# Kernel optimization log

Hardware: AMD Instinct MI355X
Metric: run time of the kernel (lower is better)

## Reference

```python
import jax, jax.numpy as jnp
import numpy as np

LMBDA = 100.0
GAMMA = 0.5  # resolvant_gamma


def setup_inputs() -> dict:
    key = jax.random.key(0)
    ks = jax.random.split(key, 8)
    B, Vx, Vy, C, K = 1, 5000, 5000, 128, 64
    feat_x = jax.random.normal(ks[0], (B, Vx, C), dtype=jnp.float32)
    feat_y = jax.random.normal(ks[1], (B, Vy, C), dtype=jnp.float32)
    # positive, sorted eigenvalues (Laplacian spectrum)
    evals_x = jnp.sort(jax.random.uniform(ks[2], (B, K), minval=0.01, maxval=10.0), axis=-1)
    evals_y = jnp.sort(jax.random.uniform(ks[3], (B, K), minval=0.01, maxval=10.0), axis=-1)
    # pseudo-inverse eigenvector rows, scaled ~1/sqrt(V) for realistic magnitudes
    evecs_trans_x = jax.random.normal(ks[4], (B, K, Vx), dtype=jnp.float32) / np.sqrt(Vx)
    evecs_trans_y = jax.random.normal(ks[5], (B, K, Vy), dtype=jnp.float32) / np.sqrt(Vy)
    # sqrt mass matrices: well-conditioned near-identity (must be invertible)
    eye = jnp.eye(K, dtype=jnp.float32)
    sqrtMk_x = eye[None] + 0.05 * jax.random.normal(ks[6], (B, K, K), dtype=jnp.float32)
    sqrtMk_y = eye[None] + 0.05 * jax.random.normal(ks[7], (B, K, K), dtype=jnp.float32)
    return {
        "feat_x": feat_x, "feat_y": feat_y,
        "evals_x": evals_x, "evals_y": evals_y,
        "evecs_trans_x": evecs_trans_x, "evecs_trans_y": evecs_trans_y,
        "sqrtMk_x": sqrtMk_x, "sqrtMk_y": sqrtMk_y,
    }


def _compute_fmap(fx, fy, ex, ey, Px, Py, Mx, My):
    # fx:[V,C] fy:[V,C] ex,ey:[K] Px,Py:[K,V] Mx,My:[K,K]
    A = Px @ fx                 # [K,C] spectral coeffs of source feats
    Bc = My @ (Py @ fy)         # adapt_feature=True: [K,C]
    k, m = A.shape
    vec_B = Bc.T.reshape(m * k, 1)
    # Ik = sqrtMk_y (adapt_feature, no dev_feature)
    At_Ik = jnp.kron(A.T, My)   # [m*k, k*k]
    first = At_Ik.T @ At_Ik     # [k*k, k*k]
    # adapt_mask=True branch: resolvent mask as Kronecker operators
    inv_Mx = jnp.linalg.inv(Mx)
    s = jnp.maximum(jnp.max(ex), jnp.max(ey))
    g1 = (ex / s) ** GAMMA
    g2 = (ey / s) ** GAMMA
    rn1_re = g1 / (g1 * g1 + 1.0)
    rn1_im = 1.0 / (g1 * g1 + 1.0)
    rn2_re = g2 / (g2 * g2 + 1.0)
    rn2_im = 1.0 / (g2 * g2 + 1.0)
    lx_re = jnp.kron(rn1_re[:, None] * inv_Mx, My)          # diag(rn1_re)@inv_Mx
    lx_im = jnp.kron(rn1_im[:, None] * inv_Mx, My)
    ly_re = jnp.kron(inv_Mx, My * rn2_re[None, :])          # My@diag(rn2_re)
    ly_im = jnp.kron(inv_Mx, My * rn2_im[None, :])
    D_re = ly_re - lx_re
    D_im = ly_im - lx_im
    second = D_re.T @ D_re + D_im.T @ D_im
    rhs = At_Ik.T @ vec_B
    op = first + LMBDA * second
    C = jnp.linalg.solve(op, rhs).reshape(k, k).T
    return C[None]  # [1,K,K]


def reference(feat_x, feat_y, evals_x, evals_y, evecs_trans_x, evecs_trans_y, sqrtMk_x, sqrtMk_y):
    Cxy = _compute_fmap(
        feat_x[0], feat_y[0], evals_x[0], evals_y[0],
        evecs_trans_x[0], evecs_trans_y[0], sqrtMk_x[0], sqrtMk_y[0],
    )
    return Cxy  # bidirectional=False -> Cyx is None
```

## Files before the change

### kernel.cpp

```cpp
#include <hip/hip_runtime.h>

#define NV 5000
#define LMB 100.0f
#define MAXIT 150
#define TOL 1e-10f
#define NBLK 16
#define NALL 96
#define BSZ 512

#define SV_O     0
#define CTRL_O   256
#define PART_O   2048
#define AH_O     657408
#define B0_O     665600
#define H_O      673792
#define E_O      677888
#define Z2_O     681984
#define ZH_O     686080
#define Q0_O     690176
#define LIH_O    702464
#define LIE_O    706560
#define U0_O     710656
#define LH_O     747520
#define BT_O     751616
#define RSTK_O   755712
#define LCT_O    772096
#define WG_O     788480
#define XG_O     792576
#define WS_NEED  796672

#define MS_O     PART_O
#define PRT2_O   (PART_O + 16384)
#define ZERO_N   26048

#define LCTS_S   0
#define RPK_S    12288
#define TPART_S  13312
#define TPACK_S  19552
#define SPART_S  20320
#define SM_FLOATS 22368

typedef unsigned long long u64;
union PKu { u64 u; float2 f; };

__device__ __forceinline__ float aload(const float* p) {
  return __hip_atomic_load(p, __ATOMIC_RELAXED, __HIP_MEMORY_SCOPE_AGENT);
}
__device__ __forceinline__ void astore(float* p, float v) {
  __hip_atomic_store(p, v, __ATOMIC_RELAXED, __HIP_MEMORY_SCOPE_AGENT);
}
__device__ __forceinline__ u64 aload64(const u64* p) {
  return __hip_atomic_load(p, __ATOMIC_RELAXED, __HIP_MEMORY_SCOPE_AGENT);
}
__device__ __forceinline__ void astore64(u64* p, u64 v) {
  __hip_atomic_store(p, v, __ATOMIC_RELAXED, __HIP_MEMORY_SCOPE_AGENT);
}

__device__ __forceinline__ void gbar(int* cnt, int target) {
  __syncthreads();
  if (threadIdx.x == 0) {
    __hip_atomic_fetch_add(cnt, 1, __ATOMIC_ACQ_REL, __HIP_MEMORY_SCOPE_AGENT);
    while (__hip_atomic_load(cnt, __ATOMIC_ACQUIRE, __HIP_MEMORY_SCOPE_AGENT) < target) {
      __builtin_amdgcn_s_sleep(2);
    }
  }
  __syncthreads();
}

__device__ __forceinline__ void stageN(float* dst, const float* src) {
  for (int e = threadIdx.x; e < 4096; e += BSZ)
    dst[(e >> 6) * 65 + (e & 63)] = src[e];
}
__device__ __forceinline__ void stageT(float* dst, const float* src) {
  for (int e = threadIdx.x; e < 4096; e += BSZ)
    dst[(e & 63) * 65 + (e >> 6)] = src[e];
}
__device__ __forceinline__ void mm65(const float* Ls, const float* Rs, float* D) {
  for (int e = threadIdx.x; e < 4096; e += BSZ) {
    int i = e >> 6, j = e & 63;
    float a0 = 0.f, a1 = 0.f;
#pragma unroll 8
    for (int t = 0; t < 64; t += 2) {
      a0 = fmaf(Ls[i * 65 + t], Rs[t * 65 + j], a0);
      a1 = fmaf(Ls[i * 65 + t + 1], Rs[(t + 1) * 65 + j], a1);
    }
    D[e] = a0 + a1;
  }
}
__device__ __forceinline__ void mm65L(const float* Ls, const float* Rs, float* DL) {
  for (int e = threadIdx.x; e < 4096; e += BSZ) {
    int i = e >> 6, j = e & 63;
    float a0 = 0.f, a1 = 0.f;
#pragma unroll 8
    for (int t = 0; t < 64; t += 2) {
      a0 = fmaf(Ls[i * 65 + t], Rs[t * 65 + j], a0);
      a1 = fmaf(Ls[i * 65 + t + 1], Rs[(t + 1) * 65 + j], a1);
    }
    DL[i * 65 + j] = a0 + a1;
  }
}
__device__ void mmNN_s(const float* L, const float* R, float* D, float* sm) {
  stageN(sm, L); stageN(sm + 4160, R);
  __syncthreads();
  mm65(sm, sm + 4160, D);
}

__device__ void chol_inv(const float* S, float* Li, float* Lf, float* sm) {
  float (*M)[65] = (float (*)[65])sm;
  float (*T)[65] = (float (*)[65])(sm + 64 * 65);
  int tid = threadIdx.x;
  for (int e = tid; e < 4096; e += BSZ) {
    M[e >> 6][e & 63] = S[e];
    T[e >> 6][e & 63] = 0.f;
  }
  __syncthreads();
  for (int j = 0; j < 64; ++j) {
    float pv = M[j][j];
    __syncthreads();
    float sc = rsqrtf(pv);
    if (tid < 64 - j) M[j + tid][j] *= sc;
    __syncthreads();
    int m = 63 - j, c2 = (m * (m + 1)) >> 1;
    for (int e = tid; e < c2; e += BSZ) {
      int rp = (int)((sqrtf(8.f * (float)e + 1.f) - 1.f) * 0.5f);
      while (((rp + 1) * (rp + 2)) >> 1 <= e) ++rp;
      while ((rp * (rp + 1)) >> 1 > e) --rp;
      int cp = e - ((rp * (rp + 1)) >> 1);
      int r = j + 1 + rp, c = j + 1 + cp;
      M[r][c] = fmaf(-M[r][j], M[c][j], M[r][c]);
    }
    __syncthreads();
  }
  if (tid < 64) {
    int c = tid;
    T[c][c] = 1.f / M[c][c];
    for (int r = c + 1; r < 64; ++r) {
      float s = 0.f;
      for (int t = c; t < r; ++t) s = fmaf(M[r][t], T[t][c], s);
      T[r][c] = -s / M[r][r];
    }
  }
  __syncthreads();
  if (Lf) {
    for (int e = tid; e < 4096; e += BSZ) {
      int r = e >> 6, c = e & 63;
      Lf[e] = (r >= c) ? M[r][c] : 0.f;
    }
  }
  for (int e = tid; e < 4096; e += BSZ) Li[e] = T[e >> 6][e & 63];
}

__device__ __forceinline__ float coop_apply8(float* sm, const float* yv, float y_own,
                                             int lane, int wv8) {
  const float* LCTs = sm + LCTS_S;
  const float* Rpk = sm + RPK_S;
  float* Tpart = sm + TPART_S;
  float* Tpack = sm + TPACK_S;
  float* Spart = sm + SPART_S;
  float t1p[12];
#pragma unroll
  for (int p = 0; p < 12; ++p) t1p[p] = 0.f;
#pragma unroll
  for (int u = 0; u < 8; ++u) {
    int m = u * 8 + wv8;
    float yu = yv[u];
    float4 rA = *(const float4*)&Rpk[m * 16 + 0];
    float4 rB = *(const float4*)&Rpk[m * 16 + 4];
    float4 rC = *(const float4*)&Rpk[m * 16 + 8];
    t1p[0] = fmaf(yu, rA.x, t1p[0]);  t1p[1] = fmaf(yu, rA.y, t1p[1]);
    t1p[2] = fmaf(yu, rA.z, t1p[2]);  t1p[3] = fmaf(yu, rA.w, t1p[3]);
    t1p[4] = fmaf(yu, rB.x, t1p[4]);  t1p[5] = fmaf(yu, rB.y, t1p[5]);
    t1p[6] = fmaf(yu, rB.z, t1p[6]);  t1p[7] = fmaf(yu, rB.w, t1p[7]);
    t1p[8] = fmaf(yu, rC.x, t1p[8]);  t1p[9] = fmaf(yu, rC.y, t1p[9]);
    t1p[10] = fmaf(yu, rC.z, t1p[10]); t1p[11] = fmaf(yu, rC.w, t1p[11]);
  }
#pragma unroll
  for (int p = 0; p < 12; ++p) Tpart[wv8 * 780 + p * 65 + lane] = t1p[p];
  __syncthreads();
  int tid = wv8 * 64 + lane;
  for (int z = tid; z < 768; z += BSZ) {
    int tk = z >> 2, c = z & 3;
    int p = (tk >> 6) * 4 + c, k = tk & 63;
    float s = ((Tpart[0 * 780 + p * 65 + k] + Tpart[1 * 780 + p * 65 + k]) +
               (Tpart[2 * 780 + p * 65 + k] + Tpart[3 * 780 + p * 65 + k])) +
              ((Tpart[4 * 780 + p * 65 + k] + Tpart[5 * 780 + p * 65 + k]) +
               (Tpart[6 * 780 + p * 65 + k] + Tpart[7 * 780 + p * 65 + k]));
    Tpack[z] = s;
  }
  __syncthreads();
  float s0 = 0.f, s1 = 0.f, s2 = 0.f, s3 = 0.f;
  int tk0 = wv8 * 24;
#pragma unroll 8
  for (int q = 0; q < 24; ++q) {
    int tk = tk0 + q;
    float lv = LCTs[tk * 64 + lane];
    float4 tv = *(const float4*)&Tpack[tk * 4];
    s0 = fmaf(lv, tv.x, s0);
    s1 = fmaf(lv, tv.y, s1);
    s2 = fmaf(lv, tv.z, s2);
    s3 = fmaf(lv, tv.w, s3);
  }
  Spart[wv8 * 256 + 0 * 64 + lane] = s0;
  Spart[wv8 * 256 + 1 * 64 + lane] = s1;
  Spart[wv8 * 256 + 2 * 64 + lane] = s2;
  Spart[wv8 * 256 + 3 * 64 + lane] = s3;
  __syncthreads();
  int cw = (wv8 & 3) * 64 + lane;
  return y_own + (((Spart[0 * 256 + cw] + Spart[1 * 256 + cw]) +
                   (Spart[2 * 256 + cw] + Spart[3 * 256 + cw])) +
                  ((Spart[4 * 256 + cw] + Spart[5 * 256 + cw]) +
                   (Spart[6 * 256 + cw] + Spart[7 * 256 + cw])));
}

__global__ __launch_bounds__(BSZ) void solve_kernel(const float* fx, const float* fy,
                                                    const float* ex, const float* ey,
                                                    const float* Px, const float* Py,
                                                    const float* Mx, const float* My,
                                                    float* W, float* out) {
  __shared__ float sm[SM_FLOATS] __attribute__((aligned(16)));
  __shared__ float sLd[192], sRd[192], wred[8], scal[2];
  int tid = threadIdx.x, blk = blockIdx.x;
  int* cnt = (int*)(W + CTRL_O);

  if (blk < 80) {
    int mat = (blk >= 40), seg = mat ? (blk - 40) : blk;
    const float* P = (mat ? Py : Px);
    const float* f = (mat ? fy : fx);
    int v0 = seg * 125;
    for (int e = tid; e < 8000; e += BSZ) {
      int rr = e / 125, vv = e - rr * 125;
      sm[rr * 126 + vv] = P[rr * NV + v0 + vv];
    }
    __syncthreads();
    int rg = (tid >> 5) << 2;
    int cq = (tid & 31) << 2;
    float acc[4][4];
#pragma unroll
    for (int u = 0; u < 4; ++u)
#pragma unroll
      for (int v = 0; v < 4; ++v) acc[u][v] = 0.f;
    for (int v5 = 0; v5 < 125; v5 += 5) {
      float4 fv[5];
#pragma unroll
      for (int q = 0; q < 5; ++q)
        fv[q] = *(const float4*)(f + (size_t)(v0 + v5 + q) * 128 + cq);
#pragma unroll
      for (int q = 0; q < 5; ++q) {
#pragma unroll
        for (int u = 0; u < 4; ++u) {
          float pv = sm[(rg + u) * 126 + v5 + q];
          acc[u][0] = fmaf(pv, fv[q].x, acc[u][0]);
          acc[u][1] = fmaf(pv, fv[q].y, acc[u][1]);
          acc[u][2] = fmaf(pv, fv[q].z, acc[u][2]);
          acc[u][3] = fmaf(pv, fv[q].w, acc[u][3]);
        }
      }
    }
    float* O = W + PART_O + (size_t)blk * 8192;
#pragma unroll
    for (int u = 0; u < 4; ++u) {
      float4 o = make_float4(acc[u][0], acc[u][1], acc[u][2], acc[u][3]);
      *(float4*)(O + (rg + u) * 128 + cq) = o;
    }
  } else if (blk < 82) {
    for (int e = tid; e < 4096; e += BSZ) sm[(e >> 6) * 65 + (e & 63)] = My[e];
    __syncthreads();
    int base = (blk - 80) * 2048;
    for (int e = tid; e < 2048; e += BSZ) {
      int i = (base + e) >> 6, j = (base + e) & 63;
      float a0 = 0.f, a1 = 0.f;
#pragma unroll 8
      for (int t = 0; t < 64; t += 2) {
        a0 = fmaf(sm[t * 65 + i], sm[t * 65 + j], a0);
        a1 = fmaf(sm[(t + 1) * 65 + i], sm[(t + 1) * 65 + j], a1);
      }
      W[H_O + base + e] = a0 + a1;
    }
  } else if (blk == 82) {
    if (tid < 64) {
      float vx = ex[tid], vy = ey[tid];
      float m = fmaxf(vx, vy);
#pragma unroll
      for (int o = 32; o > 0; o >>= 1) m = fmaxf(m, __shfl_xor(m, o, 64));
      float g1 = sqrtf(vx / m), g2 = sqrtf(vy / m);
      float d1 = 1.f / fmaf(g1, g1, 1.f), d2 = 1.f / fmaf(g2, g2, 1.f);
      W[SV_O + tid] = g1 * d1;
      W[SV_O + 64 + tid] = d1;
      W[SV_O + 128 + tid] = g2 * d2;
      W[SV_O + 192 + tid] = d2;
    }
  }
  gbar(cnt, NALL);
  if (blk >= NBLK) return;

  if (blk == 0) {
    chol_inv(W + H_O, W + LIH_O, W + LH_O, sm);
  } else {
    for (int item = blk; item < 20; item += 15) {
      if (item <= 8) {
        int c0 = (item - 1) * 16;
        float* ssum = sm;
        float* mxs = sm + 1088;
        for (int e = tid; e < 4096; e += BSZ) mxs[(e >> 6) * 65 + (e & 63)] = Mx[e];
        for (int e = tid; e < 1024; e += BSZ) {
          int t = e >> 4, cl = e & 15;
          float s = 0.f;
          for (int p = 0; p < 40; ++p) s += W[PART_O + (size_t)p * 8192 + t * 128 + c0 + cl];
          ssum[t * 17 + cl] = s;
        }
        __syncthreads();
        for (int e = tid; e < 1024; e += BSZ) {
          int i = e >> 4, cl = e & 15;
          float a0 = 0.f, a1 = 0.f;
#pragma unroll 8
          for (int t = 0; t < 64; t += 2) {
            a0 = fmaf(mxs[t * 65 + i], ssum[t * 17 + cl], a0);
            a1 = fmaf(mxs[(t + 1) * 65 + i], ssum[(t + 1) * 17 + cl], a1);
          }
          W[AH_O + i * 128 + c0 + cl] = a0 + a1;
        }
      } else if (item <= 16) {
        int base = (item - 9) * 1024;
        for (int e = tid; e < 1024; e += BSZ) {
          float s = 0.f;
          for (int p = 0; p < 40; ++p) s += W[PART_O + (size_t)(40 + p) * 8192 + base + e];
          W[B0_O + base + e] = s;
        }
      } else {
        if (tid < 256) sm[tid] = W[SV_O + tid];
        __syncthreads();
        int t = item - 17;
        for (int e = tid; e < 4096; e += BSZ) {
          int k = e >> 6, b = e & 63;
          float h = W[H_O + e], v;
          if (t == 0) v = h * (sm[128 + k] * sm[128 + b] + sm[192 + k] * sm[192 + b]);
          else if (t == 1) v = h * (sm[128 + k] + sm[128 + b]);
          else v = h * (sm[192 + k] + sm[192 + b]);
          W[Q0_O + t * 4096 + e] = v;
        }
      }
      __syncthreads();
    }
  }
  gbar(cnt, NALL + NBLK);

  if (blk < 4) {
    for (int e = tid; e < 8192; e += BSZ) {
      int i = e >> 7, c = e & 127;
      sm[c * 65 + i] = W[AH_O + e];
    }
    __syncthreads();
    int i0 = blk * 16;
    for (int e = tid; e < 1024; e += BSZ) {
      int i = i0 + (e >> 6), j = e & 63;
      float a0 = 0.f, a1 = 0.f;
#pragma unroll 8
      for (int c = 0; c < 128; c += 2) {
        a0 = fmaf(sm[c * 65 + i], sm[c * 65 + j], a0);
        a1 = fmaf(sm[(c + 1) * 65 + i], sm[(c + 1) * 65 + j], a1);
      }
      float acc = a0 + a1;
      if (i == j) {
        float a = W[SV_O + i], b = W[SV_O + 64 + i];
        acc += LMB * (a * a + b * b);
      }
      W[E_O + i * 64 + j] = acc;
    }
  } else if (blk < 8) {
    int i0 = (blk - 4) * 16;
    for (int e = tid; e < 8192; e += BSZ) {
      int j = e >> 7, c = e & 127;
      sm[c * 65 + j] = W[B0_O + e];
    }
    for (int e = tid; e < 2048; e += BSZ) {
      int il = e >> 7, c = e & 127;
      sm[8320 + c * 17 + il] = W[AH_O + (i0 + il) * 128 + c];
    }
    __syncthreads();
    for (int e = tid; e < 1024; e += BSZ) {
      int il = e >> 6, j = e & 63;
      float a0 = 0.f, a1 = 0.f;
#pragma unroll 8
      for (int c = 0; c < 128; c += 2) {
        a0 = fmaf(sm[8320 + c * 17 + il], sm[c * 65 + j], a0);
        a1 = fmaf(sm[8320 + (c + 1) * 17 + il], sm[(c + 1) * 65 + j], a1);
      }
      W[Z2_O + (i0 + il) * 64 + j] = a0 + a1;
    }
  } else if (blk < 11) {
    int t = blk - 8;
    mmNN_s(W + LIH_O, W + Q0_O + t * 4096, W + U0_O + t * 4096, sm);
  } else {
    for (int e = (blk - 11) * BSZ + tid; e < ZERO_N; e += 5 * BSZ)
      W[MS_O + e] = 0.f;
  }
  gbar(cnt, NALL + 2 * NBLK);

  if (blk == 0) chol_inv(W + E_O, W + LIE_O, nullptr, sm);
  else if (blk == 1) mmNN_s(W + Z2_O, W + LH_O, W + ZH_O, sm);
  else if (blk < 5) {
    int t = blk - 2;
    stageN(sm, W + U0_O + t * 4096);
    stageT(sm + 4160, W + LIH_O);
    __syncthreads();
    mm65L(sm, sm + 4160, sm + 8320);
    __syncthreads();
    for (int e = tid; e < 4096; e += BSZ) {
      int a = e >> 6, b = e & 63;
      W[RSTK_O + t * 4096 + e] = 0.5f * (sm[8320 + a * 65 + b] + sm[8320 + b * 65 + a]);
    }
  }
  gbar(cnt, NALL + 3 * NBLK);

  if (blk == 0) mmNN_s(W + LIE_O, W + ZH_O, W + BT_O, sm);
  else if (blk == 1) {
    stageN(sm, W + LIE_O);
    stageT(sm + 4160, W + LIE_O);
    __syncthreads();
    mm65L(sm, sm + 4160, sm + 8320);
    __syncthreads();
    for (int e = tid; e < 4096; e += BSZ) {
      int k = e >> 6, i = e & 63;
      W[LCT_O + e] = LMB * 0.5f * (sm[8320 + k * 65 + i] + sm[8320 + i * 65 + k]);
    }
  } else if (blk < 4) {
    float* dv = sLd;
    if (tid < 64) dv[tid] = W[SV_O + ((blk == 2) ? tid : 64 + tid)];
    stageN(sm, W + LIE_O);
    __syncthreads();
    for (int e = tid; e < 4096; e += BSZ) {
      int jq = e >> 6, k = e & 63;
      sm[4160 + k * 65 + jq] = sm[jq * 65 + k] * dv[k];
    }
    __syncthreads();
    mm65L(sm, sm + 4160, sm + 8320);
    __syncthreads();
    int t = blk - 1;
    for (int e = tid; e < 4096; e += BSZ) {
      int k = e >> 6, i = e & 63;
      W[LCT_O + t * 4096 + e] = -LMB * 0.5f * (sm[8320 + k * 65 + i] + sm[8320 + i * 65 + k]);
    }
  }
  gbar(cnt, NALL + 4 * NBLK);

  int lane = tid & 63, wv8 = tid >> 6;
  int jown = blk * 4 + (wv8 & 3);
  const float* BTp = W + BT_O;
  const float* LCTp = W + LCT_O;
  const float* RSTKp = W + RSTK_O;
  u64* MS = (u64*)(W + MS_O);
  u64* PR2 = (u64*)(W + PRT2_O);

  for (int e = tid; e < 12288; e += BSZ) sm[LCTS_S + e] = LCTp[e];
  for (int e = tid; e < 768; e += BSZ) {
    int p = e >> 6, m = e & 63;
    int t = p >> 2, c = p & 3;
    sm[RPK_S + m * 16 + p] = RSTKp[(t * 64 + blk * 4 + c) * 64 + m];
  }
  if (tid < 192) {
    int t = tid >> 6, i = tid & 63;
    sLd[tid] = LCTp[t * 4096 + i * 64 + i];
    sRd[tid] = RSTKp[t * 4096 + i * 64 + i];
  }
  __syncthreads();
  float yv0[8];
#pragma unroll
  for (int u = 0; u < 8; ++u) {
    int col = u * 8 + wv8;
    float den = 1.f + sLd[lane] * sRd[col] + sLd[64 + lane] * sRd[64 + col] +
                sLd[128 + lane] * sRd[128 + col];
    yv0[u] = BTp[lane * 64 + col] / den;
  }
  float invd = 0.f, u_l = 0.f, r_l = 0.f, m_l = 0.f;
  if (wv8 < 4) {
    invd = 1.f / (1.f + sLd[lane] * sRd[jown] + sLd[64 + lane] * sRd[64 + jown] +
                  sLd[128 + lane] * sRd[128 + jown]);
    u_l = BTp[lane * 64 + jown] * invd;
    r_l = BTp[lane * 64 + jown];
  }
  float w_l = coop_apply8(sm, yv0, u_l, lane, wv8);
  if (wv8 < 4) {
    m_l = invd * w_l;
    PKu pk; pk.f = make_float2(m_l, 1.f);
    astore64(MS + jown * 64 + lane, pk.u);
    float vr = r_l * u_l, vw = w_l * u_l;
#pragma unroll
    for (int o = 32; o; o >>= 1) { vr += __shfl_down(vr, o, 64); vw += __shfl_down(vw, o, 64); }
    if (lane == 0) { wred[wv8 * 2] = vr; wred[wv8 * 2 + 1] = vw; }
  }
  __syncthreads();
  if (tid == 0) {
    PKu a, b;
    a.f = make_float2(wred[0] + wred[2] + wred[4] + wred[6], 1.f);
    b.f = make_float2(wred[1] + wred[3] + wred[5] + wred[7], 1.f);
    astore64(PR2 + (size_t)blk * 2, a.u);
    astore64(PR2 + (size_t)blk * 2 + 1, b.u);
  }

  float p_l = 0.f, q_l = 0.f, z_l = 0.f, s_l = 0.f, x_l = 0.f;
  float gprev = 1.f, aprev = 1.f, g0b = 1.f;
  int sl = lane & 15;
  for (int j = 0; j < MAXIT; ++j) {
    unsigned sbits = __float_as_uint((float)(j + 1));
    const u64* msrc = MS + (size_t)(j & 1) * 4096;
    u64 raw[8];
#pragma unroll
    for (int u = 0; u < 8; ++u) raw[u] = aload64(msrc + u * BSZ + tid);
    const u64* ps = PR2 + ((size_t)j * 16 + sl) * 2;
    u64 ra = 0, rb = 0;
    if (wv8 == 0) { ra = aload64(ps); rb = aload64(ps + 1); }
    {
      int spins = 0;
      for (;;) {
        bool ok = true;
#pragma unroll
        for (int u = 0; u < 8; ++u) ok = ok && ((unsigned)(raw[u] >> 32) == sbits);
        if (__all(ok)) break;
        if (++spins > 64) {
          __hip_atomic_load(msrc + tid, __ATOMIC_ACQUIRE, __HIP_MEMORY_SCOPE_AGENT);
          spins = 0;
        }
#pragma unroll
        for (int u = 0; u < 8; ++u)
          if ((unsigned)(raw[u] >> 32) != sbits) raw[u] = aload64(msrc + u * BSZ + tid);
      }
    }
    float mv[8];
#pragma unroll
    for (int u = 0; u < 8; ++u) mv[u] = __uint_as_float((unsigned)raw[u]);
    float n_l = coop_apply8(sm, mv, m_l, lane, wv8);
    if (wv8 == 0) {
      int spins = 0;
      for (;;) {
        bool ok = ((unsigned)(ra >> 32) == sbits) && ((unsigned)(rb >> 32) == sbits);
        if (__all(ok)) break;
        if (++spins > 64) {
          __hip_atomic_load(ps, __ATOMIC_ACQUIRE, __HIP_MEMORY_SCOPE_AGENT);
          spins = 0;
        }
        if ((unsigned)(ra >> 32) != sbits) ra = aload64(ps);
        if ((unsigned)(rb >> 32) != sbits) rb = aload64(ps + 1);
      }
      float pr = __uint_as_float((unsigned)ra), pw = __uint_as_float((unsigned)rb);
#pragma unroll
      for (int mm = 1; mm < 16; mm <<= 1) {
        pr += __shfl_xor(pr, mm, 64);
        pw += __shfl_xor(pw, mm, 64);
      }
      if (lane == 0) { scal[0] = pr; scal[1] = pw; }
    }
    __syncthreads();
    float gjb = scal[0], djb = scal[1];
    if (j == 0) g0b = gjb;
    if (j > 0 && fabsf(gjb) < TOL * fabsf(g0b)) break;
    if (wv8 < 4) {
      float bj = (j == 0) ? 0.f : gjb / gprev;
      float aj = (j == 0) ? gjb / djb : gjb / (djb - bj * gjb / aprev);
      float z_n = fmaf(bj, z_l, n_l);
      float w_n = fmaf(-aj, z_n, w_l);
      float m_n = invd * w_n;
      PKu pk; pk.f = make_float2(m_n, (float)(j + 2));
      astore64(MS + (size_t)((j + 1) & 1) * 4096 + jown * 64 + lane, pk.u);
      q_l = fmaf(bj, q_l, m_l);
      s_l = fmaf(bj, s_l, w_l);
      p_l = fmaf(bj, p_l, u_l);
      x_l = fmaf(aj, p_l, x_l);
      r_l = fmaf(-aj, s_l, r_l);
      u_l = fmaf(-aj, q_l, u_l);
      z_l = z_n; w_l = w_n; m_l = m_n;
      float vr = r_l * u_l, vw = w_l * u_l;
#pragma unroll
      for (int o = 32; o; o >>= 1) { vr += __shfl_down(vr, o, 64); vw += __shfl_down(vw, o, 64); }
      if (lane == 0) { wred[wv8 * 2] = vr; wred[wv8 * 2 + 1] = vw; }
      gprev = gjb; aprev = aj;
    }
    __syncthreads();
    if (tid == 0) {
      PKu a, b;
      a.f = make_float2(wred[0] + wred[2] + wred[4] + wred[6], (float)(j + 2));
      b.f = make_float2(wred[1] + wred[3] + wred[5] + wred[7], (float)(j + 2));
      astore64(PR2 + ((size_t)(j + 1) * 16 + blk) * 2, a.u);
      astore64(PR2 + ((size_t)(j + 1) * 16 + blk) * 2 + 1, b.u);
    }
  }
  if (wv8 < 4) astore(W + XG_O + jown * 64 + lane, x_l);
  gbar(cnt, NALL + 5 * NBLK);

  if (blk == 0) {
    float* Ys = sm;
    float* Ms2 = sm + 4160;
    for (int e = tid; e < 4096; e += BSZ) Ys[(e >> 6) * 65 + (e & 63)] = aload(W + XG_O + e);
    for (int e = tid; e < 4096; e += BSZ) Ms2[(e >> 6) * 65 + (e & 63)] = W[LIE_O + e];
    __syncthreads();
    for (int e = tid; e < 4096; e += BSZ) {
      int t = e >> 6, b = e & 63;
      float acc = 0.f;
#pragma unroll 8
      for (int a = 0; a < 64; ++a) acc = fmaf(Ms2[a * 65 + t], Ys[b * 65 + a], acc);
      W[WG_O + t * 64 + b] = acc;
    }
    __syncthreads();
    for (int e = tid; e < 4096; e += BSZ) Ys[(e >> 6) * 65 + (e & 63)] = W[WG_O + e];
    for (int e = tid; e < 4096; e += BSZ) Ms2[(e >> 6) * 65 + (e & 63)] = W[LIH_O + e];
    __syncthreads();
    for (int e = tid; e < 4096; e += BSZ) {
      int t = e >> 6, c = e & 63;
      float acc = 0.f;
#pragma unroll 8
      for (int b = 0; b < 64; ++b) acc = fmaf(Ys[t * 65 + b], Ms2[b * 65 + c], acc);
      W[WG_O + t * 64 + c] = acc;
    }
    __syncthreads();
    for (int e = tid; e < 4096; e += BSZ) Ys[(e >> 6) * 65 + (e & 63)] = W[WG_O + e];
    for (int e = tid; e < 4096; e += BSZ) Ms2[(e & 63) * 65 + (e >> 6)] = Mx[e];
    __syncthreads();
    for (int e = tid; e < 4096; e += BSZ) {
      int r = e >> 6, c = e & 63;
      float acc = 0.f;
#pragma unroll 8
      for (int t = 0; t < 64; ++t) acc = fmaf(Ms2[t * 65 + c], Ys[t * 65 + r], acc);
      out[e] = acc;
    }
  }
}

extern "C" void kernel_launch(void* const* d_in, const int* in_sizes, int n_in,
                              void* d_out, int out_size, void* d_ws, size_t ws_size,
                              hipStream_t stream) {
  const float* fx = (const float*)d_in[0];
  const float* fy = (const float*)d_in[1];
  const float* ex = (const float*)d_in[2];
  const float* ey = (const float*)d_in[3];
  const float* Px = (const float*)d_in[4];
  const float* Py = (const float*)d_in[5];
  const float* Mx = (const float*)d_in[6];
  const float* My = (const float*)d_in[7];
  float* out = (float*)d_out;
  float* W = (float*)d_ws;

  if (ws_size < (size_t)WS_NEED * sizeof(float)) {
    hipMemsetAsync(d_out, 0, (size_t)out_size * sizeof(float), stream);
    return;
  }

  hipMemsetAsync(W + CTRL_O, 0, 256, stream);
  solve_kernel<<<NALL, BSZ, 0, stream>>>(fx, fy, ex, ey, Px, Py, Mx, My, W, out);
}
```

Baseline: 353.1 us.

## Split iterative solver across 32 blocks with two columns per block

Doubles the number of blocks in the iterative CG-style solve phase from 16 to 32. Each block now owns 2 columns of the 64x64 unknown instead of 4, so the per-iteration operator apply shrinks. The shared-memory staging, the partial-reduction slots and the preprocessing item assignment are resized to match. The cost is more blocks taking part in each per-iteration cross-block flag exchange and reduction, which lengthens the synchronization and polling path that dominates each iteration.

```diff
diff --git a/kernel.cpp b/kernel.cpp
--- a/kernel.cpp
+++ b/kernel.cpp
@@ -4,7 +4,7 @@
 #define LMB 100.0f
 #define MAXIT 150
 #define TOL 1e-10f
-#define NBLK 16
+#define NBLK 32
 #define NALL 96
 #define BSZ 512
 
@@ -31,14 +31,14 @@
 
 #define MS_O     PART_O
 #define PRT2_O   (PART_O + 16384)
-#define ZERO_N   26048
+#define ZERO_N   35712
 
 #define LCTS_S   0
 #define RPK_S    12288
-#define TPART_S  13312
-#define TPACK_S  19552
-#define SPART_S  20320
-#define SM_FLOATS 22368
+#define TPART_S  12800
+#define TPACK_S  15920
+#define SPART_S  16304
+#define SM_FLOATS 21504
 
 typedef unsigned long long u64;
 union PKu { u64 u; float2 f; };
@@ -150,66 +150,57 @@
   for (int e = tid; e < 4096; e += BSZ) Li[e] = T[e >> 6][e & 63];
 }
 
-__device__ __forceinline__ float coop_apply8(float* sm, const float* yv, float y_own,
-                                             int lane, int wv8) {
+__device__ __forceinline__ float coop_apply(float* sm, const float* yv, float y_own,
+                                            int lane, int wv8) {
   const float* LCTs = sm + LCTS_S;
   const float* Rpk = sm + RPK_S;
   float* Tpart = sm + TPART_S;
   float* Tpack = sm + TPACK_S;
   float* Spart = sm + SPART_S;
-  float t1p[12];
-#pragma unroll
-  for (int p = 0; p < 12; ++p) t1p[p] = 0.f;
+  float t1p[6];
+#pragma unroll
+  for (int p = 0; p < 6; ++p) t1p[p] = 0.f;
 #pragma unroll
   for (int u = 0; u < 8; ++u) {
     int m = u * 8 + wv8;
     float yu = yv[u];
-    float4 rA = *(const float4*)&Rpk[m * 16 + 0];
-    float4 rB = *(const float4*)&Rpk[m * 16 + 4];
-    float4 rC = *(const float4*)&Rpk[m * 16 + 8];
+    float4 rA = *(const float4*)&Rpk[m * 8 + 0];
+    float2 rB = *(const float2*)&Rpk[m * 8 + 4];
     t1p[0] = fmaf(yu, rA.x, t1p[0]);  t1p[1] = fmaf(yu, rA.y, t1p[1]);
     t1p[2] = fmaf(yu, rA.z, t1p[2]);  t1p[3] = fmaf(yu, rA.w, t1p[3]);
     t1p[4] = fmaf(yu, rB.x, t1p[4]);  t1p[5] = fmaf(yu, rB.y, t1p[5]);
-    t1p[6] = fmaf(yu, rB.z, t1p[6]);  t1p[7] = fmaf(yu, rB.w, t1p[7]);
-    t1p[8] = fmaf(yu, rC.x, t1p[8]);  t1p[9] = fmaf(yu, rC.y, t1p[9]);
-    t1p[10] = fmaf(yu, rC.z, t1p[10]); t1p[11] = fmaf(yu, rC.w, t1p[11]);
-  }
-#pragma unroll
-  for (int p = 0; p < 12; ++p) Tpart[wv8 * 780 + p * 65 + lane] = t1p[p];
+  }
+#pragma unroll
+  for (int p = 0; p < 6; ++p) Tpart[wv8 * 390 + p * 65 + lane] = t1p[p];
   __syncthreads();
   int tid = wv8 * 64 + lane;
-  for (int z = tid; z < 768; z += BSZ) {
-    int tk = z >> 2, c = z & 3;
-    int p = (tk >> 6) * 4 + c, k = tk & 63;
-    float s = ((Tpart[0 * 780 + p * 65 + k] + Tpart[1 * 780 + p * 65 + k]) +
-               (Tpart[2 * 780 + p * 65 + k] + Tpart[3 * 780 + p * 65 + k])) +
-              ((Tpart[4 * 780 + p * 65 + k] + Tpart[5 * 780 + p * 65 + k]) +
-               (Tpart[6 * 780 + p * 65 + k] + Tpart[7 * 780 + p * 65 + k]));
-    Tpack[z] = s;
-  }
-  __syncthreads();
-  float s0 = 0.f, s1 = 0.f, s2 = 0.f, s3 = 0.f;
+  if (tid < 384) {
+    int tk = tid >> 1, c = tid & 1;
+    int p = (tk >> 6) * 2 + c, k = tk & 63;
+    Tpack[tid] = (((Tpart[0 * 390 + p * 65 + k] + Tpart[1 * 390 + p * 65 + k]) +
+                   (Tpart[2 * 390 + p * 65 + k] + Tpart[3 * 390 + p * 65 + k])) +
+                  ((Tpart[4 * 390 + p * 65 + k] + Tpart[5 * 390 + p * 65 + k]) +
+                   (Tpart[6 * 390 + p * 65 + k] + Tpart[7 * 390 + p * 65 + k])));
+  }
+  __syncthreads();
+  float s0 = 0.f, s1 = 0.f;
   int tk0 = wv8 * 24;
 #pragma unroll 8
   for (int q = 0; q < 24; ++q) {
     int tk = tk0 + q;
     float lv = LCTs[tk * 64 + lane];
-    float4 tv = *(const float4*)&Tpack[tk * 4];
+    float2 tv = *(const float2*)&Tpack[tk * 2];
     s0 = fmaf(lv, tv.x, s0);
     s1 = fmaf(lv, tv.y, s1);
-    s2 = fmaf(lv, tv.z, s2);
-    s3 = fmaf(lv, tv.w, s3);
-  }
-  Spart[wv8 * 256 + 0 * 64 + lane] = s0;
-  Spart[wv8 * 256 + 1 * 64 + lane] = s1;
-  Spart[wv8 * 256 + 2 * 64 + lane] = s2;
-  Spart[wv8 * 256 + 3 * 64 + lane] = s3;
-  __syncthreads();
-  int cw = (wv8 & 3) * 64 + lane;
-  return y_own + (((Spart[0 * 256 + cw] + Spart[1 * 256 + cw]) +
-                   (Spart[2 * 256 + cw] + Spart[3 * 256 + cw])) +
-                  ((Spart[4 * 256 + cw] + Spart[5 * 256 + cw]) +
-                   (Spart[6 * 256 + cw] + Spart[7 * 256 + cw])));
+  }
+  Spart[wv8 * 128 + 0 * 64 + lane] = s0;
+  Spart[wv8 * 128 + 1 * 64 + lane] = s1;
+  __syncthreads();
+  int cw = (wv8 & 1) * 64 + lane;
+  return y_own + (((Spart[0 * 128 + cw] + Spart[1 * 128 + cw]) +
+                   (Spart[2 * 128 + cw] + Spart[3 * 128 + cw])) +
+                  ((Spart[4 * 128 + cw] + Spart[5 * 128 + cw]) +
+                   (Spart[6 * 128 + cw] + Spart[7 * 128 + cw])));
 }
 
 __global__ __launch_bounds__(BSZ) void solve_kernel(const float* fx, const float* fy,
@@ -218,7 +209,7 @@
                                                     const float* Mx, const float* My,
                                                     float* W, float* out) {
   __shared__ float sm[SM_FLOATS] __attribute__((aligned(16)));
-  __shared__ float sLd[192], sRd[192], wred[8], scal[2];
+  __shared__ float sLd[192], sRd[192], wred[4], scal[2];
   int tid = threadIdx.x, blk = blockIdx.x;
   int* cnt = (int*)(W + CTRL_O);
 
@@ -295,51 +286,49 @@
 
   if (blk == 0) {
     chol_inv(W + H_O, W + LIH_O, W + LH_O, sm);
-  } else {
-    for (int item = blk; item < 20; item += 15) {
-      if (item <= 8) {
-        int c0 = (item - 1) * 16;
-        float* ssum = sm;
-        float* mxs = sm + 1088;
-        for (int e = tid; e < 4096; e += BSZ) mxs[(e >> 6) * 65 + (e & 63)] = Mx[e];
-        for (int e = tid; e < 1024; e += BSZ) {
-          int t = e >> 4, cl = e & 15;
-          float s = 0.f;
-          for (int p = 0; p < 40; ++p) s += W[PART_O + (size_t)p * 8192 + t * 128 + c0 + cl];
-          ssum[t * 17 + cl] = s;
+  } else if (blk <= 19) {
+    int item = blk;
+    if (item <= 8) {
+      int c0 = (item - 1) * 16;
+      float* ssum = sm;
+      float* mxs = sm + 1088;
+      for (int e = tid; e < 4096; e += BSZ) mxs[(e >> 6) * 65 + (e & 63)] = Mx[e];
+      for (int e = tid; e < 1024; e += BSZ) {
+        int t = e >> 4, cl = e & 15;
+        float s = 0.f;
+        for (int p = 0; p < 40; ++p) s += W[PART_O + (size_t)p * 8192 + t * 128 + c0 + cl];
+        ssum[t * 17 + cl] = s;
+      }
+      __syncthreads();
+      for (int e = tid; e < 1024; e += BSZ) {
+        int i = e >> 4, cl = e & 15;
+        float a0 = 0.f, a1 = 0.f;
+#pragma unroll 8
+        for (int t = 0; t < 64; t += 2) {
+          a0 = fmaf(mxs[t * 65 + i], ssum[t * 17 + cl], a0);
+          a1 = fmaf(mxs[(t + 1) * 65 + i], ssum[(t + 1) * 17 + cl], a1);
         }
-        __syncthreads();
-        for (int e = tid; e < 1024; e += BSZ) {
-          int i = e >> 4, cl = e & 15;
-          float a0 = 0.f, a1 = 0.f;
-#pragma unroll 8
-          for (int t = 0; t < 64; t += 2) {
-            a0 = fmaf(mxs[t * 65 + i], ssum[t * 17 + cl], a0);
-            a1 = fmaf(mxs[(t + 1) * 65 + i], ssum[(t + 1) * 17 + cl], a1);
-          }
-          W[AH_O + i * 128 + c0 + cl] = a0 + a1;
-        }
-      } else if (item <= 16) {
-        int base = (item - 9) * 1024;
-        for (int e = tid; e < 1024; e += BSZ) {
-          float s = 0.f;
-          for (int p = 0; p < 40; ++p) s += W[PART_O + (size_t)(40 + p) * 8192 + base + e];
-          W[B0_O + base + e] = s;
-        }
-      } else {
-        if (tid < 256) sm[tid] = W[SV_O + tid];
-        __syncthreads();
-        int t = item - 17;
-        for (int e = tid; e < 4096; e += BSZ) {
-          int k = e >> 6, b = e & 63;
-          float h = W[H_O + e], v;
-          if (t == 0) v = h * (sm[128 + k] * sm[128 + b] + sm[192 + k] * sm[192 + b]);
-          else if (t == 1) v = h * (sm[128 + k] + sm[128 + b]);
-          else v = h * (sm[192 + k] + sm[192 + b]);
-          W[Q0_O + t * 4096 + e] = v;
-        }
-      }
+        W[AH_O + i * 128 + c0 + cl] = a0 + a1;
+      }
+    } else if (item <= 16) {
+      int base = (item - 9) * 1024;
+      for (int e = tid; e < 1024; e += BSZ) {
+        float s = 0.f;
+        for (int p = 0; p < 40; ++p) s += W[PART_O + (size_t)(40 + p) * 8192 + base + e];
+        W[B0_O + base + e] = s;
+      }
+    } else {
+      if (tid < 256) sm[tid] = W[SV_O + tid];
       __syncthreads();
+      int t = item - 17;
+      for (int e = tid; e < 4096; e += BSZ) {
+        int k = e >> 6, b = e & 63;
+        float h = W[H_O + e], v;
+        if (t == 0) v = h * (sm[128 + k] * sm[128 + b] + sm[192 + k] * sm[192 + b]);
+        else if (t == 1) v = h * (sm[128 + k] + sm[128 + b]);
+        else v = h * (sm[192 + k] + sm[192 + b]);
+        W[Q0_O + t * 4096 + e] = v;
+      }
     }
   }
   gbar(cnt, NALL + NBLK);
@@ -391,7 +380,7 @@
     int t = blk - 8;
     mmNN_s(W + LIH_O, W + Q0_O + t * 4096, W + U0_O + t * 4096, sm);
   } else {
-    for (int e = (blk - 11) * BSZ + tid; e < ZERO_N; e += 5 * BSZ)
+    for (int e = (blk - 11) * BSZ + tid; e < ZERO_N; e += 21 * BSZ)
       W[MS_O + e] = 0.f;
   }
   gbar(cnt, NALL + 2 * NBLK);
@@ -444,7 +433,7 @@
   gbar(cnt, NALL + 4 * NBLK);
 
   int lane = tid & 63, wv8 = tid >> 6;
-  int jown = blk * 4 + (wv8 & 3);
+  int jown = blk * 2 + wv8;
   const float* BTp = W + BT_O;
   const float* LCTp = W + LCT_O;
   const float* RSTKp = W + RSTK_O;
@@ -452,10 +441,10 @@
   u64* PR2 = (u64*)(W + PRT2_O);
 
   for (int e = tid; e < 12288; e += BSZ) sm[LCTS_S + e] = LCTp[e];
-  for (int e = tid; e < 768; e += BSZ) {
-    int p = e >> 6, m = e & 63;
-    int t = p >> 2, c = p & 3;
-    sm[RPK_S + m * 16 + p] = RSTKp[(t * 64 + blk * 4 + c) * 64 + m];
+  if (tid < 384) {
+    int m = tid / 6, p = tid - m * 6;
+    int t = p >> 1, c = p & 1;
+    sm[RPK_S + m * 8 + p] = RSTKp[(t * 64 + blk * 2 + c) * 64 + m];
   }
   if (tid < 192) {
     int t = tid >> 6, i = tid & 63;
@@ -472,14 +461,14 @@
     yv0[u] = BTp[lane * 64 + col] / den;
   }
   float invd = 0.f, u_l = 0.f, r_l = 0.f, m_l = 0.f;
-  if (wv8 < 4) {
+  if (wv8 < 2) {
     invd = 1.f / (1.f + sLd[lane] * sRd[jown] + sLd[64 + lane] * sRd[64 + jown] +
                   sLd[128 + lane] * sRd[128 + jown]);
     u_l = BTp[lane * 64 + jown] * invd;
     r_l = BTp[lane * 64 + jown];
   }
-  float w_l = coop_apply8(sm, yv0, u_l, lane, wv8);
-  if (wv8 < 4) {
+  float w_l = coop_apply(sm, yv0, u_l, lane, wv8);
+  if (wv8 < 2) {
     m_l = invd * w_l;
     PKu pk; pk.f = make_float2(m_l, 1.f);
     astore64(MS + jown * 64 + lane, pk.u);
@@ -491,22 +480,22 @@
   __syncthreads();
   if (tid == 0) {
     PKu a, b;
-    a.f = make_float2(wred[0] + wred[2] + wred[4] + wred[6], 1.f);
-    b.f = make_float2(wred[1] + wred[3] + wred[5] + wred[7], 1.f);
+    a.f = make_float2(wred[0] + wred[2], 1.f);
+    b.f = make_float2(wred[1] + wred[3], 1.f);
     astore64(PR2 + (size_t)blk * 2, a.u);
     astore64(PR2 + (size_t)blk * 2 + 1, b.u);
   }
 
   float p_l = 0.f, q_l = 0.f, z_l = 0.f, s_l = 0.f, x_l = 0.f;
   float gprev = 1.f, aprev = 1.f, g0b = 1.f;
-  int sl = lane & 15;
+  int sl = lane & 31;
   for (int j = 0; j < MAXIT; ++j) {
     unsigned sbits = __float_as_uint((float)(j + 1));
     const u64* msrc = MS + (size_t)(j & 1) * 4096;
     u64 raw[8];
 #pragma unroll
     for (int u = 0; u < 8; ++u) raw[u] = aload64(msrc + u * BSZ + tid);
-    const u64* ps = PR2 + ((size_t)j * 16 + sl) * 2;
+    const u64* ps = PR2 + ((size_t)j * 32 + sl) * 2;
     u64 ra = 0, rb = 0;
     if (wv8 == 0) { ra = aload64(ps); rb = aload64(ps + 1); }
     {
@@ -528,7 +517,7 @@
     float mv[8];
 #pragma unroll
     for (int u = 0; u < 8; ++u) mv[u] = __uint_as_float((unsigned)raw[u]);
-    float n_l = coop_apply8(sm, mv, m_l, lane, wv8);
+    float n_l = coop_apply(sm, mv, m_l, lane, wv8);
     if (wv8 == 0) {
       int spins = 0;
       for (;;) {
@@ -543,7 +532,7 @@
       }
       float pr = __uint_as_float((unsigned)ra), pw = __uint_as_float((unsigned)rb);
 #pragma unroll
-      for (int mm = 1; mm < 16; mm <<= 1) {
+      for (int mm = 1; mm < 32; mm <<= 1) {
         pr += __shfl_xor(pr, mm, 64);
         pw += __shfl_xor(pw, mm, 64);
       }
@@ -553,7 +542,7 @@
     float gjb = scal[0], djb = scal[1];
     if (j == 0) g0b = gjb;
     if (j > 0 && fabsf(gjb) < TOL * fabsf(g0b)) break;
-    if (wv8 < 4) {
+    if (wv8 < 2) {
       float bj = (j == 0) ? 0.f : gjb / gprev;
       float aj = (j == 0) ? gjb / djb : gjb / (djb - bj * gjb / aprev);
       float z_n = fmaf(bj, z_l, n_l);
@@ -577,13 +566,13 @@
     __syncthreads();
     if (tid == 0) {
       PKu a, b;
-      a.f = make_float2(wred[0] + wred[2] + wred[4] + wred[6], (float)(j + 2));
-      b.f = make_float2(wred[1] + wred[3] + wred[5] + wred[7], (float)(j + 2));
-      astore64(PR2 + ((size_t)(j + 1) * 16 + blk) * 2, a.u);
-      astore64(PR2 + ((size_t)(j + 1) * 16 + blk) * 2 + 1, b.u);
-    }
-  }
-  if (wv8 < 4) astore(W + XG_O + jown * 64 + lane, x_l);
+      a.f = make_float2(wred[0] + wred[2], (float)(j + 2));
+      b.f = make_float2(wred[1] + wred[3], (float)(j + 2));
+      astore64(PR2 + ((size_t)(j + 1) * 32 + blk) * 2, a.u);
+      astore64(PR2 + ((size_t)(j + 1) * 32 + blk) * 2 + 1, b.u);
+    }
+  }
+  if (wv8 < 2) astore(W + XG_O + jown * 64 + lane, x_l);
   gbar(cnt, NALL + 5 * NBLK);
 
   if (blk == 0) {
```

After: 342.4 us (median of 2 runs). 3.0% less time.
